# Kernel optimization log

Hardware: AMD Instinct MI355X
Metric: run time of the kernel (lower is better)

Reference implementation:

```python
import jax, jax.numpy as jnp
import numpy as np

ARTIST_V = 16384
GENRE_V = 2048
TOTAL = ARTIST_V + GENRE_V + 1  # 18433
HIDDEN = TOTAL // 2            # 9216
OUT = 64
BATCH = 4096


def setup_inputs() -> dict:
    key = jax.random.key(0)
    k1, k2, k3, k4, k5, k6, k7 = jax.random.split(key, 7)
    artist_ids = jax.random.randint(k1, (BATCH,), 0, ARTIST_V, dtype=jnp.int64 if jax.config.jax_enable_x64 else jnp.int32)
    genre_ids = jax.random.randint(k2, (BATCH,), 0, GENRE_V, dtype=artist_ids.dtype)
    year_norms = jax.random.uniform(k3, (BATCH,), dtype=jnp.float32)
    s1 = 1.0 / np.sqrt(TOTAL)
    s2 = 1.0 / np.sqrt(HIDDEN)
    W1 = jax.random.uniform(k4, (HIDDEN, TOTAL), jnp.float32, -s1, s1)
    b1 = jax.random.uniform(k5, (HIDDEN,), jnp.float32, -s1, s1)
    W2 = jax.random.uniform(k6, (OUT, HIDDEN), jnp.float32, -s2, s2)
    b2 = jax.random.uniform(k7, (OUT,), jnp.float32, -s2, s2)
    return {"artist_ids": artist_ids, "genre_ids": genre_ids, "year_norms": year_norms,
            "W1": W1, "b1": b1, "W2": W2, "b2": b2}


def reference(artist_ids, genre_ids, year_norms, W1, b1, W2, b2):
    # one_hot(artist) @ W1[:, :A].T  ==  gather of W1 columns == gather of W1.T rows.
    # combined = [onehot(artist) | onehot(genre) | year] -> Linear -> ReLU -> Linear
    # (Dropout is identity at inference.)
    W1T = W1.T  # [TOTAL, HIDDEN]
    h = (W1T[artist_ids]                     # [B, HIDDEN] artist one-hot matmul
         + W1T[ARTIST_V + genre_ids]         # genre one-hot matmul
         + year_norms[:, None] * W1T[-1]     # year scalar column
         + b1)
    h = jax.nn.relu(h)
    return h @ W2.T + b2  # [B, OUT]
```

## Files before the change

kernel.cpp:

```cpp
#include <hip/hip_runtime.h>

#define ARTIST_V 16384
#define GENRE_V  2048
#define TOTAL    18433
#define HIDDEN   9216
#define OUT_D    64
#define BATCH    4096

#define ROWS_PB  8
#define NBLK     (HIDDEN / ROWS_PB)
#define THR      512
#define SEG      (TOTAL - 1)
#define PF_N     (SEG / 4 / THR)

#define KSPLIT   8
#define KCHUNK   (HIDDEN / KSPLIT)

typedef unsigned int   uint;
typedef unsigned short ushort;
typedef __attribute__((ext_vector_type(8))) short short8;
typedef __attribute__((ext_vector_type(4))) float f32x4;

__device__ __forceinline__ ushort f2bf(float f) {
    uint u = __float_as_uint(f);
    u += 0x7FFFu + ((u >> 16) & 1u);
    return (ushort)(u >> 16);
}
__device__ __forceinline__ float bf2f(ushort b) {
    return __uint_as_float(((uint)b) << 16);
}
__device__ __forceinline__ uint cvt_pk(float a, float b) {
    uint r;
    asm("v_cvt_pk_bf16_f32 %0, %1, %2" : "=v"(r) : "v"(a), "v"(b));
    return r;
}

__global__ __launch_bounds__(256) void k_prep(const float* __restrict__ W2,
                                              ushort* __restrict__ W2b) {
    int t = blockIdx.x * 256 + threadIdx.x;
    float4 v = *(const float4*)(W2 + (size_t)t * 4);
    uint2 p;
    p.x = cvt_pk(v.x, v.y);
    p.y = cvt_pk(v.z, v.w);
    *(uint2*)(W2b + (size_t)t * 4) = p;
}

__global__ __launch_bounds__(THR, 4) void k_hidden(
    const int*   __restrict__ artist,
    const int*   __restrict__ genre,
    const float* __restrict__ year,
    const float* __restrict__ W1,
    const float* __restrict__ b1,
    uint4*       __restrict__ H2v)
{
    __shared__ ushort srow[2][SEG];
    const int tid = threadIdx.x;
    const int hb  = blockIdx.x;
    const int h0  = hb * ROWS_PB;

    uint  ag[8]; float yv[8];
    #pragma unroll
    for (int j = 0; j < 8; j++) {
        int b = tid + THR * j;
        ag[j] = (uint)artist[b] | ((uint)genre[b] << 16);
        yv[j] = year[b];
    }
    float ywA[ROWS_PB], b1A[ROWS_PB];
    #pragma unroll
    for (int r = 0; r < ROWS_PB; r++) {
        ywA[r] = W1[(size_t)(h0 + r) * TOTAL + SEG];
        b1A[r] = b1[h0 + r];
    }

    uint res[8][4];
    #pragma unroll
    for (int j = 0; j < 8; j++)
        { res[j][0] = 0u; res[j][1] = 0u; res[j][2] = 0u; res[j][3] = 0u; }

    float4 pf[PF_N];
    {
        const float4* vp = (const float4*)(W1 + (size_t)h0 * TOTAL);
        #pragma unroll
        for (int i = 0; i < PF_N; i++) pf[i] = vp[i * THR + tid];
        #pragma unroll
        for (int i = 0; i < PF_N; i++) {
            uint2 p; p.x = cvt_pk(pf[i].x, pf[i].y); p.y = cvt_pk(pf[i].z, pf[i].w);
            *(uint2*)(&srow[0][(i * THR + tid) * 4]) = p;
        }
        __syncthreads();
    }

    #pragma unroll
    for (int r = 0; r < ROWS_PB; r++) {
        if (r + 1 < ROWS_PB) {
            const float4* vp = (const float4*)(W1 + (size_t)(h0 + r + 1) * TOTAL);
            #pragma unroll
            for (int i = 0; i < PF_N; i++) pf[i] = vp[i * THR + tid];
        }
        const ushort* sr = srow[r & 1];
        const float yw = ywA[r], bh = b1A[r];
        #pragma unroll
        for (int j = 0; j < 8; j++) {
            int a = (int)(ag[j] & 0xFFFFu);
            int g = (int)(ag[j] >> 16);
            float hv = bf2f(sr[a]) + bf2f(sr[ARTIST_V + g]) + yv[j] * yw + bh;
            hv = fmaxf(hv, 0.0f);
            res[j][r >> 1] |= ((uint)f2bf(hv)) << ((r & 1) * 16);
        }
        if (r + 1 < ROWS_PB) {
            ushort* sw = srow[(r + 1) & 1];
            #pragma unroll
            for (int i = 0; i < PF_N; i++) {
                uint2 p; p.x = cvt_pk(pf[i].x, pf[i].y); p.y = cvt_pk(pf[i].z, pf[i].w);
                *(uint2*)(&sw[(i * THR + tid) * 4]) = p;
            }
            __syncthreads();
        }
    }

    const size_t obase = (size_t)hb * BATCH;
    #pragma unroll
    for (int j = 0; j < 8; j++) {
        uint4 v; v.x = res[j][0]; v.y = res[j][1]; v.z = res[j][2]; v.w = res[j][3];
        H2v[obase + tid + THR * j] = v;
    }
}

__global__ __launch_bounds__(256, 2) void k_gemm(
    const uint4*  __restrict__ H2v,
    const ushort* __restrict__ W2b,
    float*        __restrict__ part)
{
    const int lane = threadIdx.x & 63;
    const int wv   = threadIdx.x >> 6;
    const int l15  = lane & 15;
    const int lhi  = lane >> 4;
    const int m0   = blockIdx.x * 64 + wv * 16;
    const int k0   = blockIdx.y * KCHUNK;

    f32x4 acc[4];
    #pragma unroll
    for (int n = 0; n < 4; n++) acc[n] = (f32x4){0.f, 0.f, 0.f, 0.f};

    uint4 avn = H2v[(size_t)((k0 >> 3) + lhi) * BATCH + m0 + l15];
    for (int kk = k0; kk < k0 + KCHUNK; kk += 32) {
        uint4 av = avn;
        if (kk + 32 < k0 + KCHUNK)
            avn = H2v[(size_t)(((kk + 32) >> 3) + lhi) * BATCH + m0 + l15];
        union { uint4 u; short8 s; } ua; ua.u = av;
        short8 afrag = ua.s;

        const ushort* wb = W2b + (size_t)l15 * HIDDEN + kk + lhi * 8;
        #pragma unroll
        for (int n = 0; n < 4; n++) {
            short8 bfrag = *(const short8*)(wb + (size_t)(n * 16) * HIDDEN);
            acc[n] = __builtin_amdgcn_mfma_f32_16x16x32_bf16(afrag, bfrag, acc[n], 0, 0, 0);
        }
    }

    float* pb = part + (size_t)blockIdx.y * (BATCH * OUT_D);
    #pragma unroll
    for (int n = 0; n < 4; n++) {
        #pragma unroll
        for (int r = 0; r < 4; r++)
            pb[(size_t)(m0 + lhi * 4 + r) * OUT_D + n * 16 + l15] = acc[n][r];
    }
}

__global__ __launch_bounds__(256) void k_reduce(const float* __restrict__ part,
                                                const float* __restrict__ b2,
                                                float4*      __restrict__ out4) {
    int idx = blockIdx.x * 256 + threadIdx.x;
    const float4* p = (const float4*)part;
    float4 bb = ((const float4*)b2)[threadIdx.x & 15];
    float4 o = bb;
    #pragma unroll
    for (int s = 0; s < KSPLIT; s++) {
        float4 v = p[idx + (size_t)s * 65536];
        o.x += v.x; o.y += v.y; o.z += v.z; o.w += v.w;
    }
    out4[idx] = o;
}

extern "C" void kernel_launch(void* const* d_in, const int* in_sizes, int n_in,
                              void* d_out, int out_size, void* d_ws, size_t ws_size,
                              hipStream_t stream) {
    const int*   artist = (const int*)d_in[0];
    const int*   genre  = (const int*)d_in[1];
    const float* year   = (const float*)d_in[2];
    const float* W1     = (const float*)d_in[3];
    const float* b1     = (const float*)d_in[4];
    const float* W2     = (const float*)d_in[5];
    const float* b2     = (const float*)d_in[6];
    float* out = (float*)d_out;

    char* ws = (char*)d_ws;
    uint4*  H2v  = (uint4*)ws;
    ushort* W2b  = (ushort*)(ws + 75497472);
    float*  part = (float*)(ws + 75497472 + 1179648);

    k_prep  <<<576, 256, 0, stream>>>(W2, W2b);
    k_hidden<<<NBLK, THR, 0, stream>>>(artist, genre, year, W1, b1, H2v);
    k_gemm  <<<dim3(BATCH / 64, KSPLIT), 256, 0, stream>>>(H2v, W2b, part);
    k_reduce<<<256, 256, 0, stream>>>(part, b2, (float4*)out);
}
```

Baseline: 957.7 us.

## Stream W1 rows into LDS via direct global-to-LDS DMA with 36 rows per block

The hidden kernel now copies each fp32 W1 row straight into LDS with global_load_lds instead of loading it into registers, converting to bf16 and storing it. Each block handles 36 rows, giving 256 blocks, and the hidden layout changes to 4-row uint2 groups; the GEMM A-fragment load is adapted to read two uint2 per lane. The aim is to cut register pressure and the VALU conversion work in the streaming phase. The cost is fp32 LDS buffers of about 147KB, which leaves one block per CU, and fewer blocks overall, which can reduce latency hiding and load balance.

```diff
diff --git a/kernel.cpp b/kernel.cpp
--- a/kernel.cpp
+++ b/kernel.cpp
@@ -7,11 +7,9 @@
 #define OUT_D    64
 #define BATCH    4096
 
-#define ROWS_PB  8
-#define NBLK     (HIDDEN / ROWS_PB)
 #define THR      512
-#define SEG      (TOTAL - 1)
-#define PF_N     (SEG / 4 / THR)
+#define RPB      36
+#define SEG      18432
 
 #define KSPLIT   8
 #define KCHUNK   (HIDDEN / KSPLIT)
@@ -21,18 +19,18 @@
 typedef __attribute__((ext_vector_type(8))) short short8;
 typedef __attribute__((ext_vector_type(4))) float f32x4;
 
-__device__ __forceinline__ ushort f2bf(float f) {
-    uint u = __float_as_uint(f);
-    u += 0x7FFFu + ((u >> 16) & 1u);
-    return (ushort)(u >> 16);
-}
-__device__ __forceinline__ float bf2f(ushort b) {
-    return __uint_as_float(((uint)b) << 16);
-}
 __device__ __forceinline__ uint cvt_pk(float a, float b) {
     uint r;
     asm("v_cvt_pk_bf16_f32 %0, %1, %2" : "=v"(r) : "v"(a), "v"(b));
     return r;
+}
+
+__device__ __forceinline__ void dma_row(const float* __restrict__ g, float* l) {
+    #pragma unroll
+    for (int i = 0; i < 36; ++i)
+        __builtin_amdgcn_global_load_lds(
+            (const __attribute__((address_space(1))) void*)(g + i * 64),
+            (__attribute__((address_space(3))) void*)(l + i * 64), 4, 0, 0);
 }
 
 __global__ __launch_bounds__(256) void k_prep(const float* __restrict__ W2,
@@ -45,89 +43,69 @@
     *(uint2*)(W2b + (size_t)t * 4) = p;
 }
 
-__global__ __launch_bounds__(THR, 4) void k_hidden(
+__global__ __launch_bounds__(THR) void k_hidden(
     const int*   __restrict__ artist,
     const int*   __restrict__ genre,
     const float* __restrict__ year,
     const float* __restrict__ W1,
     const float* __restrict__ b1,
-    uint4*       __restrict__ H2v)
+    uint2*       __restrict__ H2)
 {
-    __shared__ ushort srow[2][SEG];
-    const int tid = threadIdx.x;
-    const int hb  = blockIdx.x;
-    const int h0  = hb * ROWS_PB;
+    __shared__ float sbuf[2][SEG];
+    const int tid  = threadIdx.x;
+    const int w    = tid >> 6;
+    const int ln   = tid & 63;
+    const int woff = w * (SEG / 8);
+    const int r0   = blockIdx.x * RPB;
 
-    uint  ag[8]; float yv[8];
+    int aix[8], gix[8]; float yv[8];
     #pragma unroll
-    for (int j = 0; j < 8; j++) {
+    for (int j = 0; j < 8; ++j) {
         int b = tid + THR * j;
-        ag[j] = (uint)artist[b] | ((uint)genre[b] << 16);
-        yv[j] = year[b];
-    }
-    float ywA[ROWS_PB], b1A[ROWS_PB];
-    #pragma unroll
-    for (int r = 0; r < ROWS_PB; r++) {
-        ywA[r] = W1[(size_t)(h0 + r) * TOTAL + SEG];
-        b1A[r] = b1[h0 + r];
+        aix[j] = artist[b];
+        gix[j] = ARTIST_V + genre[b];
+        yv[j]  = year[b];
     }
 
-    uint res[8][4];
-    #pragma unroll
-    for (int j = 0; j < 8; j++)
-        { res[j][0] = 0u; res[j][1] = 0u; res[j][2] = 0u; res[j][3] = 0u; }
+    dma_row(W1 + (size_t)r0 * TOTAL + woff + ln, &sbuf[0][woff]);
+    __syncthreads();
 
-    float4 pf[PF_N];
-    {
-        const float4* vp = (const float4*)(W1 + (size_t)h0 * TOTAL);
+    for (int m = 0; m < RPB / 4; ++m) {
+        const int rb = 4 * m;
+        const float4 bq = *(const float4*)(b1 + r0 + rb);
+        float hvp[8];
+        uint  pk0[8], pk1[8];
         #pragma unroll
-        for (int i = 0; i < PF_N; i++) pf[i] = vp[i * THR + tid];
-        #pragma unroll
-        for (int i = 0; i < PF_N; i++) {
-            uint2 p; p.x = cvt_pk(pf[i].x, pf[i].y); p.y = cvt_pk(pf[i].z, pf[i].w);
-            *(uint2*)(&srow[0][(i * THR + tid) * 4]) = p;
-        }
-        __syncthreads();
-    }
-
-    #pragma unroll
-    for (int r = 0; r < ROWS_PB; r++) {
-        if (r + 1 < ROWS_PB) {
-            const float4* vp = (const float4*)(W1 + (size_t)(h0 + r + 1) * TOTAL);
+        for (int s = 0; s < 4; ++s) {
+            const int r = rb + s;
+            if (r + 1 < RPB)
+                dma_row(W1 + (size_t)(r0 + r + 1) * TOTAL + woff + ln,
+                        &sbuf[(s + 1) & 1][woff]);
+            const float yw = W1[(size_t)(r0 + r) * TOTAL + SEG];
+            const float bh = (s == 0) ? bq.x : (s == 1) ? bq.y : (s == 2) ? bq.z : bq.w;
+            const float* sb = sbuf[s & 1];
             #pragma unroll
-            for (int i = 0; i < PF_N; i++) pf[i] = vp[i * THR + tid];
-        }
-        const ushort* sr = srow[r & 1];
-        const float yw = ywA[r], bh = b1A[r];
-        #pragma unroll
-        for (int j = 0; j < 8; j++) {
-            int a = (int)(ag[j] & 0xFFFFu);
-            int g = (int)(ag[j] >> 16);
-            float hv = bf2f(sr[a]) + bf2f(sr[ARTIST_V + g]) + yv[j] * yw + bh;
-            hv = fmaxf(hv, 0.0f);
-            res[j][r >> 1] |= ((uint)f2bf(hv)) << ((r & 1) * 16);
-        }
-        if (r + 1 < ROWS_PB) {
-            ushort* sw = srow[(r + 1) & 1];
-            #pragma unroll
-            for (int i = 0; i < PF_N; i++) {
-                uint2 p; p.x = cvt_pk(pf[i].x, pf[i].y); p.y = cvt_pk(pf[i].z, pf[i].w);
-                *(uint2*)(&sw[(i * THR + tid) * 4]) = p;
+            for (int j = 0; j < 8; ++j) {
+                float hv = sb[aix[j]] + sb[gix[j]] + fmaf(yv[j], yw, bh);
+                hv = fmaxf(hv, 0.0f);
+                if (s & 1) {
+                    uint p = cvt_pk(hvp[j], hv);
+                    if (s == 1) pk0[j] = p; else pk1[j] = p;
+                } else {
+                    hvp[j] = hv;
+                }
             }
             __syncthreads();
         }
-    }
-
-    const size_t obase = (size_t)hb * BATCH;
-    #pragma unroll
-    for (int j = 0; j < 8; j++) {
-        uint4 v; v.x = res[j][0]; v.y = res[j][1]; v.z = res[j][2]; v.w = res[j][3];
-        H2v[obase + tid + THR * j] = v;
+        const size_t qb = (size_t)(blockIdx.x * (RPB / 4) + m) * BATCH;
+        #pragma unroll
+        for (int j = 0; j < 8; ++j)
+            H2[qb + tid + THR * j] = make_uint2(pk0[j], pk1[j]);
     }
 }
 
 __global__ __launch_bounds__(256, 2) void k_gemm(
-    const uint4*  __restrict__ H2v,
+    const uint2*  __restrict__ H2,
     const ushort* __restrict__ W2b,
     float*        __restrict__ part)
 {
@@ -142,12 +120,19 @@
     #pragma unroll
     for (int n = 0; n < 4; n++) acc[n] = (f32x4){0.f, 0.f, 0.f, 0.f};
 
-    uint4 avn = H2v[(size_t)((k0 >> 3) + lhi) * BATCH + m0 + l15];
+    int p = (k0 >> 2) + lhi * 2;
+    uint2 a0 = H2[(size_t)p * BATCH + m0 + l15];
+    uint2 a1 = H2[(size_t)(p + 1) * BATCH + m0 + l15];
+
     for (int kk = k0; kk < k0 + KCHUNK; kk += 32) {
-        uint4 av = avn;
-        if (kk + 32 < k0 + KCHUNK)
-            avn = H2v[(size_t)(((kk + 32) >> 3) + lhi) * BATCH + m0 + l15];
-        union { uint4 u; short8 s; } ua; ua.u = av;
+        uint2 c0 = a0, c1 = a1;
+        if (kk + 32 < k0 + KCHUNK) {
+            int pn = ((kk + 32) >> 2) + lhi * 2;
+            a0 = H2[(size_t)pn * BATCH + m0 + l15];
+            a1 = H2[(size_t)(pn + 1) * BATCH + m0 + l15];
+        }
+        union { uint u[4]; short8 s; } ua;
+        ua.u[0] = c0.x; ua.u[1] = c0.y; ua.u[2] = c1.x; ua.u[3] = c1.y;
         short8 afrag = ua.s;
 
         const ushort* wb = W2b + (size_t)l15 * HIDDEN + kk + lhi * 8;
@@ -195,12 +180,12 @@
     float* out = (float*)d_out;
 
     char* ws = (char*)d_ws;
-    uint4*  H2v  = (uint4*)ws;
+    uint2*  H2   = (uint2*)ws;
     ushort* W2b  = (ushort*)(ws + 75497472);
     float*  part = (float*)(ws + 75497472 + 1179648);
 
     k_prep  <<<576, 256, 0, stream>>>(W2, W2b);
-    k_hidden<<<NBLK, THR, 0, stream>>>(artist, genre, year, W1, b1, H2v);
-    k_gemm  <<<dim3(BATCH / 64, KSPLIT), 256, 0, stream>>>(H2v, W2b, part);
+    k_hidden<<<256, THR, 0, stream>>>(artist, genre, year, W1, b1, H2);
+    k_gemm  <<<dim3(BATCH / 64, KSPLIT), 256, 0, stream>>>(H2, W2b, part);
     k_reduce<<<256, 256, 0, stream>>>(part, b2, (float4*)out);
 }
```

Measured after the change: 930.6 us. 1.03x faster.
